# Optimization experiments

Hardware: AMD Instinct MI355X
Metric: run time of the kernel (lower is better)

Reference implementation:

```python
import jax, jax.numpy as jnp
import numpy as np

B, Q, K, DQ, DK = 4, 256, 1024, 256, 256


def setup_inputs() -> dict:
    key = jax.random.key(0)
    ks = jax.random.split(key, 7)
    q = jax.random.normal(ks[0], (B, Q, DQ), dtype=jnp.float32)
    k = jax.random.normal(ks[1], (B, K, DK), dtype=jnp.float32)
    v = jax.random.normal(ks[2], (B, K, DK), dtype=jnp.float32)
    mask = jax.random.randint(ks[3], (B, K), 0, 2).astype(bool)
    # torch Linear(in,out,bias=False): y = x @ W.T ; store as [in,out] for einsum
    Wq = jax.random.normal(ks[4], (DQ, DK), dtype=jnp.float32) / np.sqrt(DQ)
    Wk = jax.random.normal(ks[5], (DK, DK), dtype=jnp.float32) / np.sqrt(DK)
    wv = jax.random.normal(ks[6], (DK,), dtype=jnp.float32) / np.sqrt(DK)
    return {"q": q, "k": k, "v": v, "mask": mask, "Wq": Wq, "Wk": Wk, "wv": wv}


def reference(q, k, v, mask, Wq, Wk, wv):
    # Additive (Bahdanau) attention. Original redundantly projects repeated
    # copies; projecting once then broadcasting is the same math.
    qp = jnp.einsum('bqd,de->bqe', q, Wq)          # [B,Q,DK]
    kp = jnp.einsum('bkd,de->bke', k, Wk)          # [B,K,DK]
    h = jnp.tanh(qp[:, :, None, :] + kp[:, None, :, :])  # [B,Q,K,DK]
    scores = jnp.einsum('bqke,e->bqk', h, wv)      # [B,Q,K]
    scores = jnp.where(mask[:, None, :], scores, -jnp.inf)
    probs = jax.nn.softmax(scores, axis=-1)        # [B,Q,K]
    attended = jnp.einsum('bqk,bkd->bqd', probs, v)
    return attended
```

## Files before the change

### kernel.cpp

```cpp
#include <hip/hip_runtime.h>
#include <hip/hip_bf16.h>

#define B_ 4
#define Q_ 256
#define K_ 1024
#define D_ 256
#define NVPAD 768
#define LOG2E 1.44269504f

__device__ __forceinline__ float fexp2(float x) {
    float r; asm("v_exp_f32 %0, %1" : "=v"(r) : "v"(x)); return r;
}
__device__ __forceinline__ float frcp(float x) {
    float r; asm("v_rcp_f32 %0, %1" : "=v"(r) : "v"(x)); return r;
}

__global__ void compact_kernel(const int* __restrict__ mask,
                               ushort* __restrict__ kidx,
                               int* __restrict__ nvalid) {
    const int b = blockIdx.x, lane = threadIdx.x;
    const int* m = mask + b * K_;
    const int base = lane * 16;
    int cnt = 0;
#pragma unroll
    for (int i = 0; i < 16; ++i) cnt += (m[base + i] != 0);
    int inc = cnt;
#pragma unroll
    for (int d = 1; d < 64; d <<= 1) {
        int tt = __shfl_up(inc, d);
        if (lane >= d) inc += tt;
    }
    const int total = __shfl(inc, 63);
    int pos = inc - cnt;
    ushort* kb = kidx + b * K_;
    for (int i = 0; i < 16; ++i) {
        int kk = base + i;
        if (m[kk] != 0) kb[pos++] = (ushort)kk;
    }
    for (int j = total + lane; j < K_; j += 64) kb[j] = 0;
    if (lane == 0) nvalid[b] = total;
}

__global__ __launch_bounds__(256) void proj_kernel(const float* __restrict__ q,
                                                   const float* __restrict__ k,
                                                   const float* __restrict__ Wq,
                                                   const float* __restrict__ Wk,
                                                   const ushort* __restrict__ kidx,
                                                   const int* __restrict__ nvalid,
                                                   float* __restrict__ qpE,
                                                   float* __restrict__ kpC,
                                                   float scale) {
    const int t = threadIdx.x;
    const bool isQ = blockIdx.x < 16;
    const float* A; const float* W; int m0, b = 0, nv = 0;
    __shared__ ushort s_row[64];
    if (isQ) { A = q; W = Wq; m0 = blockIdx.x * 64; }
    else {
        const int g = (blockIdx.x - 16) * 64;
        b = g >> 10;
        m0 = g & 1023;
        nv = nvalid[b];
        if (m0 >= nv) return;
        A = k; W = Wk;
        if (t < 64) s_row[t] = kidx[b * K_ + m0 + t];
    }

    __shared__ float As[16][65];
    __shared__ float Ws[16][64];
    const int tx = t & 15, ty = t >> 4;
    const int n0 = blockIdx.y * 64;
    const int ar = t >> 2, ac = (t & 3) * 4;
    const int wr = t >> 4, wc = (t & 15) * 4;
    float c[4][4] = {};
    if (!isQ) __syncthreads();
    for (int kb = 0; kb < 256; kb += 16) {
        __syncthreads();
        {
            const int src = isQ ? (m0 + ar) : (b * K_ + s_row[ar]);
            float4 av = *(const float4*)(A + (size_t)src * 256 + kb + ac);
            As[ac + 0][ar] = av.x; As[ac + 1][ar] = av.y;
            As[ac + 2][ar] = av.z; As[ac + 3][ar] = av.w;
        }
        float4 wvv = *(const float4*)(W + (size_t)(kb + wr) * 256 + n0 + wc);
        wvv.x *= scale; wvv.y *= scale; wvv.z *= scale; wvv.w *= scale;
        *(float4*)(&Ws[wr][wc]) = wvv;
        __syncthreads();
#pragma unroll
        for (int kk = 0; kk < 16; ++kk) {
            float4 bv = *(const float4*)(&Ws[kk][tx * 4]);
#pragma unroll
            for (int i = 0; i < 4; ++i) {
                float a = As[kk][ty * 4 + i];
                c[i][0] = fmaf(a, bv.x, c[i][0]);
                c[i][1] = fmaf(a, bv.y, c[i][1]);
                c[i][2] = fmaf(a, bv.z, c[i][2]);
                c[i][3] = fmaf(a, bv.w, c[i][3]);
            }
        }
    }
    if (isQ) {
#pragma unroll
        for (int i = 0; i < 4; ++i) {
            float4 o = make_float4(fexp2(c[i][0]), fexp2(c[i][1]),
                                   fexp2(c[i][2]), fexp2(c[i][3]));
            *(float4*)(qpE + (size_t)(m0 + ty * 4 + i) * 256 + n0 + tx * 4) = o;
        }
    } else {
        float* kpCb = kpC + (size_t)b * 64 * NVPAD * 4;
        const int e4 = (n0 + tx * 4) >> 2;
#pragma unroll
        for (int i = 0; i < 4; ++i) {
            const int sl = m0 + ty * 4 + i;
            if (sl < nv) {
                float4 o = make_float4(fexp2(c[i][0]), fexp2(c[i][1]),
                                       fexp2(c[i][2]), fexp2(c[i][3]));
                *(float4*)(kpCb + ((size_t)e4 * NVPAD + sl) * 4) = o;
            }
        }
    }
}

__global__ __launch_bounds__(1024, 2) void attn_kernel(const float* __restrict__ qpE,
                                                       const float* __restrict__ kpC,
                                                       const float* __restrict__ v,
                                                       const ushort* __restrict__ kidx_g,
                                                       const int* __restrict__ nvalid_g,
                                                       const float* __restrict__ wv,
                                                       float* __restrict__ out) {
    __shared__ float  s_sc[2][1024];
    __shared__ ushort s_kidx[1024];
    __shared__ float4 s_pv[32][64];
    __shared__ float  s_inv[2];

    const int tid  = threadIdx.x;
    const int lane = tid & 63;
    const int wave = tid >> 6;
    const int sl8  = lane & 7;
    const int ec   = lane >> 3;

    int bid = blockIdx.x;
    bid = (bid & 7) * 64 + (bid >> 3);
    const int b  = bid >> 7;
    const int qi = bid & 127;
    const int q0 = qi * 2;
    const int nv = nvalid_g[b];
    const int iters = (nv + 127) >> 7;

    s_kidx[tid] = (tid < nv) ? kidx_g[b * K_ + tid] : (ushort)0;
    ((float2*)s_sc)[tid] = make_float2(0.f, 0.f);
    __syncthreads();

    const float4* Bp  = (const float4*)kpC + (size_t)b * 64 * NVPAD;
    const float*  A0g = qpE + ((size_t)(b * Q_ + q0) << 8);
    const float*  A1g = A0g + 256;

    for (int eq = 0; eq < 4; ++eq) {
        const int e0 = eq * 64 + ec * 8;
        float A0[8], A1[8], W[8];
        {
            float4 x0 = *(const float4*)(A0g + e0);
            float4 x1 = *(const float4*)(A0g + e0 + 4);
            A0[0]=x0.x; A0[1]=x0.y; A0[2]=x0.z; A0[3]=x0.w;
            A0[4]=x1.x; A0[5]=x1.y; A0[6]=x1.z; A0[7]=x1.w;
            float4 y0 = *(const float4*)(A1g + e0);
            float4 y1 = *(const float4*)(A1g + e0 + 4);
            A1[0]=y0.x; A1[1]=y0.y; A1[2]=y0.z; A1[3]=y0.w;
            A1[4]=y1.x; A1[5]=y1.y; A1[6]=y1.z; A1[7]=y1.w;
            float4 w0 = *(const float4*)(wv + e0);
            float4 w1 = *(const float4*)(wv + e0 + 4);
            W[0]=w0.x; W[1]=w0.y; W[2]=w0.z; W[3]=w0.w;
            W[4]=w1.x; W[5]=w1.y; W[6]=w1.z; W[7]=w1.w;
        }
        const float4* BpE = Bp + (size_t)(eq * 16 + ec * 2) * NVPAD;

#pragma unroll 2
        for (int i = 0; i < iters; ++i) {
            const int s = i * 128 + wave * 8 + sl8;
            float4 B0 = BpE[s];
            float4 B1 = BpE[NVPAD + s];
            float a0 = 0.f, a1 = 0.f;
            a0 = fmaf(W[0], frcp(fmaf(A0[0], B0.x, 1.f)), a0);
            a1 = fmaf(W[0], frcp(fmaf(A1[0], B0.x, 1.f)), a1);
            a0 = fmaf(W[1], frcp(fmaf(A0[1], B0.y, 1.f)), a0);
            a1 = fmaf(W[1], frcp(fmaf(A1[1], B0.y, 1.f)), a1);
            a0 = fmaf(W[2], frcp(fmaf(A0[2], B0.z, 1.f)), a0);
            a1 = fmaf(W[2], frcp(fmaf(A1[2], B0.z, 1.f)), a1);
            a0 = fmaf(W[3], frcp(fmaf(A0[3], B0.w, 1.f)), a0);
            a1 = fmaf(W[3], frcp(fmaf(A1[3], B0.w, 1.f)), a1);
            a0 = fmaf(W[4], frcp(fmaf(A0[4], B1.x, 1.f)), a0);
            a1 = fmaf(W[4], frcp(fmaf(A1[4], B1.x, 1.f)), a1);
            a0 = fmaf(W[5], frcp(fmaf(A0[5], B1.y, 1.f)), a0);
            a1 = fmaf(W[5], frcp(fmaf(A1[5], B1.y, 1.f)), a1);
            a0 = fmaf(W[6], frcp(fmaf(A0[6], B1.z, 1.f)), a0);
            a1 = fmaf(W[6], frcp(fmaf(A1[6], B1.z, 1.f)), a1);
            a0 = fmaf(W[7], frcp(fmaf(A0[7], B1.w, 1.f)), a0);
            a1 = fmaf(W[7], frcp(fmaf(A1[7], B1.w, 1.f)), a1);
            a0 += __shfl_xor(a0, 8);  a1 += __shfl_xor(a1, 8);
            a0 += __shfl_xor(a0, 16); a1 += __shfl_xor(a1, 16);
            a0 += __shfl_xor(a0, 32); a1 += __shfl_xor(a1, 32);
            if (ec == 0 && s < nv) {
                s_sc[0][s] += a0;
                s_sc[1][s] += a1;
            }
        }
    }
    __syncthreads();

    if (wave < 2) {
        const int qq = wave;
        float mx = -3.0e38f;
        for (int j = lane; j < nv; j += 64) mx = fmaxf(mx, -2.f * s_sc[qq][j]);
#pragma unroll
        for (int off = 32; off > 0; off >>= 1) mx = fmaxf(mx, __shfl_xor(mx, off));
        float sum = 0.f;
        for (int j = lane; j < nv; j += 64) {
            float e = fexp2((-2.f * s_sc[qq][j] - mx) * LOG2E);
            s_sc[qq][j] = e;
            sum += e;
        }
#pragma unroll
        for (int off = 32; off > 0; off >>= 1) sum += __shfl_xor(sum, off);
        if (lane == 0) s_inv[qq] = frcp(sum);
    }
    __syncthreads();

    {
        const int dl = tid & 63;
        const int kq = tid >> 6;
        float4 o0 = {0, 0, 0, 0}, o1 = {0, 0, 0, 0};
        const float4* v4 = (const float4*)(v + ((size_t)b * K_ << 8));
        for (int k = kq; k < nv; k += 16) {
            int vr = s_kidx[k];
            float4 vv = v4[((size_t)vr << 6) + dl];
            float p0 = s_sc[0][k], p1 = s_sc[1][k];
            o0.x = fmaf(p0, vv.x, o0.x); o0.y = fmaf(p0, vv.y, o0.y);
            o0.z = fmaf(p0, vv.z, o0.z); o0.w = fmaf(p0, vv.w, o0.w);
            o1.x = fmaf(p1, vv.x, o1.x); o1.y = fmaf(p1, vv.y, o1.y);
            o1.z = fmaf(p1, vv.z, o1.z); o1.w = fmaf(p1, vv.w, o1.w);
        }
        s_pv[kq * 2 + 0][dl] = o0;
        s_pv[kq * 2 + 1][dl] = o1;
        __syncthreads();
        if (tid < 128) {
            const int qq = tid >> 6, c = tid & 63;
            float4 s = {0, 0, 0, 0};
#pragma unroll
            for (int g = 0; g < 16; ++g) {
                float4 x = s_pv[g * 2 + qq][c];
                s.x += x.x; s.y += x.y; s.z += x.z; s.w += x.w;
            }
            const float inv = s_inv[qq];
            s.x *= inv; s.y *= inv; s.z *= inv; s.w *= inv;
            ((float4*)out)[((size_t)(b * Q_ + q0 + qq) << 6) + c] = s;
        }
    }
}

extern "C" void kernel_launch(void* const* d_in, const int* in_sizes, int n_in,
                              void* d_out, int out_size, void* d_ws, size_t ws_size,
                              hipStream_t stream) {
    const float* q    = (const float*)d_in[0];
    const float* k    = (const float*)d_in[1];
    const float* v    = (const float*)d_in[2];
    const int*   mask = (const int*)d_in[3];
    const float* Wq   = (const float*)d_in[4];
    const float* Wk   = (const float*)d_in[5];
    const float* wv   = (const float*)d_in[6];
    float* out = (float*)d_out;

    float* qpE    = (float*)d_ws;
    float* kpC    = qpE + (size_t)B_ * Q_ * D_;
    ushort* kidx  = (ushort*)(kpC + (size_t)B_ * 64 * NVPAD * 4);
    int* nvalid   = (int*)(kidx + (size_t)B_ * K_);

    const float c2 = 2.885390082f;

    compact_kernel<<<dim3(B_), 64, 0, stream>>>(mask, kidx, nvalid);
    proj_kernel<<<dim3(80, 4), 256, 0, stream>>>(q, k, Wq, Wk, kidx, nvalid, qpE, kpC, c2);
    attn_kernel<<<dim3(512), 1024, 0, stream>>>(qpE, kpC, v, kidx, nvalid, wv, out);
}
```

Before: 66.24 us.

## Fuse mask compaction into projection and attention kernels, drop compact launch

Removes the separate single-wave-per-batch compaction kernel. Both the projection and attention kernels now recompute the prefix-sum over the mask themselves, using wave shuffles plus a shared-memory cross-wave scan. This removes one kernel launch and its serial dependency, which was a small 4-block kernel on the critical path. In exchange, every block redundantly reads the batch mask and pays a few extra barriers.

```diff
diff --git a/kernel.cpp b/kernel.cpp
--- a/kernel.cpp
+++ b/kernel.cpp
@@ -15,38 +15,11 @@
     float r; asm("v_rcp_f32 %0, %1" : "=v"(r) : "v"(x)); return r;
 }
 
-__global__ void compact_kernel(const int* __restrict__ mask,
-                               ushort* __restrict__ kidx,
-                               int* __restrict__ nvalid) {
-    const int b = blockIdx.x, lane = threadIdx.x;
-    const int* m = mask + b * K_;
-    const int base = lane * 16;
-    int cnt = 0;
-#pragma unroll
-    for (int i = 0; i < 16; ++i) cnt += (m[base + i] != 0);
-    int inc = cnt;
-#pragma unroll
-    for (int d = 1; d < 64; d <<= 1) {
-        int tt = __shfl_up(inc, d);
-        if (lane >= d) inc += tt;
-    }
-    const int total = __shfl(inc, 63);
-    int pos = inc - cnt;
-    ushort* kb = kidx + b * K_;
-    for (int i = 0; i < 16; ++i) {
-        int kk = base + i;
-        if (m[kk] != 0) kb[pos++] = (ushort)kk;
-    }
-    for (int j = total + lane; j < K_; j += 64) kb[j] = 0;
-    if (lane == 0) nvalid[b] = total;
-}
-
 __global__ __launch_bounds__(256) void proj_kernel(const float* __restrict__ q,
                                                    const float* __restrict__ k,
                                                    const float* __restrict__ Wq,
                                                    const float* __restrict__ Wk,
-                                                   const ushort* __restrict__ kidx,
-                                                   const int* __restrict__ nvalid,
+                                                   const int* __restrict__ mask,
                                                    float* __restrict__ qpE,
                                                    float* __restrict__ kpC,
                                                    float scale) {
@@ -54,15 +27,44 @@
     const bool isQ = blockIdx.x < 16;
     const float* A; const float* W; int m0, b = 0, nv = 0;
     __shared__ ushort s_row[64];
+    __shared__ int s_wtot[4], s_woff[4], s_nv4;
+
     if (isQ) { A = q; W = Wq; m0 = blockIdx.x * 64; }
     else {
         const int g = (blockIdx.x - 16) * 64;
         b = g >> 10;
         m0 = g & 1023;
-        nv = nvalid[b];
+        A = k; W = Wk;
+        const int lane64 = t & 63, wv4 = t >> 6;
+        const int* mb = mask + b * K_ + t * 4;
+        const int b0 = (mb[0] != 0), b1 = (mb[1] != 0),
+                  b2 = (mb[2] != 0), b3 = (mb[3] != 0);
+        const int m4 = b0 + b1 + b2 + b3;
+        int inc = m4;
+#pragma unroll
+        for (int d = 1; d < 64; d <<= 1) {
+            int tt = __shfl_up(inc, d);
+            if (lane64 >= d) inc += tt;
+        }
+        if (lane64 == 63) s_wtot[wv4] = inc;
+        if (t < 64) s_row[t] = 0;
+        __syncthreads();
+        if (t < 4) {
+            int off = 0;
+            for (int w = 0; w < t; ++w) off += s_wtot[w];
+            s_woff[t] = off;
+            if (t == 3) s_nv4 = off + s_wtot[3];
+        }
+        __syncthreads();
+        nv = s_nv4;
         if (m0 >= nv) return;
-        A = k; W = Wk;
-        if (t < 64) s_row[t] = kidx[b * K_ + m0 + t];
+        int pos = s_woff[wv4] + inc - m4;
+        const int kb4 = t * 4;
+        if (b0) { int sl = pos++; if (sl >= m0 && sl < m0 + 64) s_row[sl - m0] = (ushort)(kb4);     }
+        if (b1) { int sl = pos++; if (sl >= m0 && sl < m0 + 64) s_row[sl - m0] = (ushort)(kb4 + 1); }
+        if (b2) { int sl = pos++; if (sl >= m0 && sl < m0 + 64) s_row[sl - m0] = (ushort)(kb4 + 2); }
+        if (b3) { int sl = pos++; if (sl >= m0 && sl < m0 + 64) s_row[sl - m0] = (ushort)(kb4 + 3); }
+        __syncthreads();
     }
 
     __shared__ float As[16][65];
@@ -72,7 +74,6 @@
     const int ar = t >> 2, ac = (t & 3) * 4;
     const int wr = t >> 4, wc = (t & 15) * 4;
     float c[4][4] = {};
-    if (!isQ) __syncthreads();
     for (int kb = 0; kb < 256; kb += 16) {
         __syncthreads();
         {
@@ -123,14 +124,14 @@
 __global__ __launch_bounds__(1024, 2) void attn_kernel(const float* __restrict__ qpE,
                                                        const float* __restrict__ kpC,
                                                        const float* __restrict__ v,
-                                                       const ushort* __restrict__ kidx_g,
-                                                       const int* __restrict__ nvalid_g,
+                                                       const int* __restrict__ mask,
                                                        const float* __restrict__ wv,
                                                        float* __restrict__ out) {
     __shared__ float  s_sc[2][1024];
     __shared__ ushort s_kidx[1024];
     __shared__ float4 s_pv[32][64];
     __shared__ float  s_inv[2];
+    __shared__ int    s_wtot[16], s_woff[16], s_nvs;
 
     const int tid  = threadIdx.x;
     const int lane = tid & 63;
@@ -143,12 +144,30 @@
     const int b  = bid >> 7;
     const int qi = bid & 127;
     const int q0 = qi * 2;
-    const int nv = nvalid_g[b];
+
+    const int mv = (mask[b * K_ + tid] != 0) ? 1 : 0;
+    int incp = mv;
+#pragma unroll
+    for (int d = 1; d < 64; d <<= 1) {
+        int tt = __shfl_up(incp, d);
+        if (lane >= d) incp += tt;
+    }
+    if (lane == 63) s_wtot[wave] = incp;
+    s_kidx[tid] = 0;
+    ((float2*)s_sc)[tid] = make_float2(0.f, 0.f);
+    __syncthreads();
+    if (tid < 16) {
+        int off = 0;
+        for (int w = 0; w < tid; ++w) off += s_wtot[w];
+        s_woff[tid] = off;
+        if (tid == 15) s_nvs = off + s_wtot[15];
+    }
+    __syncthreads();
+    const int nv = s_nvs;
+    if (mv) s_kidx[s_woff[wave] + incp - 1] = (ushort)tid;
+    __syncthreads();
+
     const int iters = (nv + 127) >> 7;
-
-    s_kidx[tid] = (tid < nv) ? kidx_g[b * K_ + tid] : (ushort)0;
-    ((float2*)s_sc)[tid] = make_float2(0.f, 0.f);
-    __syncthreads();
 
     const float4* Bp  = (const float4*)kpC + (size_t)b * 64 * NVPAD;
     const float*  A0g = qpE + ((size_t)(b * Q_ + q0) << 8);
@@ -268,14 +287,11 @@
     const float* wv   = (const float*)d_in[6];
     float* out = (float*)d_out;
 
-    float* qpE    = (float*)d_ws;
-    float* kpC    = qpE + (size_t)B_ * Q_ * D_;
-    ushort* kidx  = (ushort*)(kpC + (size_t)B_ * 64 * NVPAD * 4);
-    int* nvalid   = (int*)(kidx + (size_t)B_ * K_);
+    float* qpE = (float*)d_ws;
+    float* kpC = qpE + (size_t)B_ * Q_ * D_;
 
     const float c2 = 2.885390082f;
 
-    compact_kernel<<<dim3(B_), 64, 0, stream>>>(mask, kidx, nvalid);
-    proj_kernel<<<dim3(80, 4), 256, 0, stream>>>(q, k, Wq, Wk, kidx, nvalid, qpE, kpC, c2);
-    attn_kernel<<<dim3(512), 1024, 0, stream>>>(qpE, kpC, v, kidx, nvalid, wv, out);
-}
+    proj_kernel<<<dim3(80, 4), 256, 0, stream>>>(q, k, Wq, Wk, mask, qpE, kpC, c2);
+    attn_kernel<<<dim3(512), 1024, 0, stream>>>(qpE, kpC, v, mask, wv, out);
+}
```

Result: faster. 60.86 us (-8.1%).
